# Optimization experiments

Measured on AMD Instinct MI355X. Metric: run time of the kernel, lower is better.

## Reference

```python
import jax, jax.numpy as jnp
import numpy as np

# TimeVaryingDelayLine forward (warmup=False path).
# The torch code builds an (N,C,T,max_delay+1) unfolded buffer and a triangular
# weight tensor relu(1 - |delay_axis - dt|). Since weights are a triangular hat of
# width 2, exactly two taps are nonzero: delay floor(dt) with weight (1-frac) and
# delay floor(dt)+1 with weight frac (frac = dt - floor(dt)). We compute the
# identical math with a direct fractional-index gather + lerp.

MAX_DELAY = 40000
CHANNELS = 2
BATCH = 8
T = 1_000_000

def setup_inputs() -> dict:
    key = jax.random.key(0)
    k1, k2 = jax.random.split(key)
    x = jax.random.normal(k1, (BATCH, CHANNELS, T), dtype=jnp.float32)
    # delays in samples, in [0, MAX_DELAY-1) so the +1 tap index stays in range
    dt = jax.random.uniform(k2, (BATCH, CHANNELS, T), dtype=jnp.float32) * (MAX_DELAY - 1)
    buffer = jnp.zeros((BATCH, CHANNELS, MAX_DELAY), dtype=jnp.float32)
    return {"x": x, "dt": dt, "buffer": buffer}

def reference(x, dt, buffer):
    max_delay = buffer.shape[2]
    n_samples = x.shape[2]
    # x_pad[..., max_delay + t] is the current sample t  -> shape (N, C, max_delay + T)
    x_pad = jnp.concatenate([buffer, x], axis=2)
    pos = max_delay + jnp.arange(n_samples, dtype=jnp.int32)  # (T,)
    i0 = jnp.floor(dt).astype(jnp.int32)          # integer part of delay
    frac = dt - i0.astype(dt.dtype)               # fractional part in [0,1)
    idx0 = pos[None, None, :] - i0                # tap at delay floor(dt)
    idx1 = jnp.maximum(idx0 - 1, 0)               # tap at delay floor(dt)+1 (clipped; weight 0 at edge)
    tap0 = jnp.take_along_axis(x_pad, idx0, axis=2)
    tap1 = jnp.take_along_axis(x_pad, idx1, axis=2)
    y = (1.0 - frac) * tap0 + frac * tap1
    return y
```

## Files before the change

kernel.cpp:

```cpp
#include <hip/hip_runtime.h>
#include <stdint.h>


#define MAX_DELAY 40000
#define T_LEN     1000000
#define XPAD      (MAX_DELAY + T_LEN)
#define CHUNK     8192
#define S_ELEMS   16384
#define S_BYTES   (S_ELEMS * 4)
#define NPASS     3
#define CPS       123
#define NXCD      8

typedef __attribute__((address_space(3))) uint32_t       lds_u32;
typedef const __attribute__((address_space(1))) uint32_t glb_u32;

__global__ __launch_bounds__(256, 2) void tvdl_kernel(
    const float* __restrict__ x,
    const float* __restrict__ dt,
    const float* __restrict__ buf,
    float* __restrict__ y,
    int chunk_per_xcd)
{
    __shared__ float lds[S_ELEMS];

    int bid = blockIdx.x;
    int lb  = (bid & (NXCD - 1)) * chunk_per_xcd + (bid >> 3);
    int nc  = lb / CPS;
    int c   = lb - nc * CPS;
    int t0  = c * CHUNK;
    int tid = threadIdx.x;

    const float* __restrict__ xs  = x   + (size_t)nc * T_LEN;
    const float* __restrict__ bs  = buf + (size_t)nc * MAX_DELAY;
    const float* __restrict__ dts = dt  + (size_t)nc * T_LEN;
    float*       __restrict__ ys  = y   + (size_t)nc * T_LEN;

    int   b1[8][4];
    float fr[8][4];
    float acc[8][4];

#pragma unroll
    for (int k = 0; k < 8; ++k) {
        int go   = (k * 256 + tid) * 4;
        int lidx = t0 + go;
        int lc   = lidx > T_LEN - 4 ? T_LEN - 4 : lidx;
        float4 d4 = *reinterpret_cast<const float4*>(dts + lc);
        float dv[4] = {d4.x, d4.y, d4.z, d4.w};
#pragma unroll
        for (int j = 0; j < 4; ++j) {
            float dvj = dv[j];
            int   i0  = (int)dvj;
            fr[k][j]  = dvj - (float)i0;
            b1[k][j]  = (MAX_DELAY - 1 + (go + j) - i0) * 4;
            acc[k][j] = 0.0f;
        }
    }

#pragma unroll
    for (int p = 0; p < NPASS; ++p) {
#pragma unroll
        for (int q = 0; q < 16; ++q) {
            int g = t0 + p * S_ELEMS + (q * 256 + tid) * 4;
            if (g > XPAD - 4) g = XPAD - 4;
            const float* src = (g >= MAX_DELAY) ? (xs + (g - MAX_DELAY))
                                                : (bs + g);
            float* dst = lds + (size_t)(q * 256 + (tid & 192)) * 4;
            __builtin_amdgcn_global_load_lds((glb_u32*)src, (lds_u32*)dst, 16, 0, 0);
        }
        __syncthreads();

#pragma unroll
        for (int k = 0; k < 8; ++k) {
#pragma unroll
            for (int j = 0; j < 4; ++j) {
                int      bb = b1[k][j] - p * S_BYTES;
                unsigned ub = (unsigned)bb;
                if (ub < (unsigned)(S_BYTES - 4)) {
                    const float* lp = (const float*)((const char*)lds + ub);
                    float t1v = lp[0];
                    float t0v = lp[1];
                    float f   = fr[k][j];
                    acc[k][j] = fmaf(1.0f - f, t0v, fmaf(f, t1v, acc[k][j]));
                } else if (ub == (unsigned)(S_BYTES - 4)) {
                    acc[k][j] = fmaf(fr[k][j], lds[S_ELEMS - 1], acc[k][j]);
                } else if (bb == -4) {
                    acc[k][j] = fmaf(1.0f - fr[k][j], lds[0], acc[k][j]);
                }
            }
        }

        if (p + 1 < NPASS) __syncthreads();
    }

#pragma unroll
    for (int k = 0; k < 8; ++k) {
        int go = (k * 256 + tid) * 4;
        if (t0 + go < T_LEN) {
            *reinterpret_cast<float4*>(ys + t0 + go) =
                make_float4(acc[k][0], acc[k][1], acc[k][2], acc[k][3]);
        }
    }
}

extern "C" void kernel_launch(void* const* d_in, const int* in_sizes, int n_in,
                              void* d_out, int out_size, void* d_ws, size_t ws_size,
                              hipStream_t stream) {
    const float* x   = (const float*)d_in[0];
    const float* dt  = (const float*)d_in[1];
    const float* buf = (const float*)d_in[2];
    float* y = (float*)d_out;

    int nseries = out_size / T_LEN;
    int blocks  = nseries * CPS;
    int chunk_per_xcd = blocks / NXCD;
    tvdl_kernel<<<blocks, 256, 0, stream>>>(x, dt, buf, y, chunk_per_xcd);
}
```

Before: 82.18 us.

## Double-buffer LDS staging to overlap next window load with tap gathering

Splits the 64KB LDS window into two 32KB buffers and doubles the number of passes to six. The next window is issued with async global-to-LDS loads while the current window is gathered and interpolated, so memory latency can hide behind LDS work. In exchange, each pass still checks all 32 taps per thread, so the per-pass bounds tests and branching double. There are also more barriers.

```diff
diff --git a/kernel.cpp b/kernel.cpp
--- a/kernel.cpp
+++ b/kernel.cpp
@@ -6,9 +6,9 @@
 #define T_LEN     1000000
 #define XPAD      (MAX_DELAY + T_LEN)
 #define CHUNK     8192
-#define S_ELEMS   16384
+#define S_ELEMS   8192
 #define S_BYTES   (S_ELEMS * 4)
-#define NPASS     3
+#define NPASS     6
 #define CPS       123
 #define NXCD      8
 
@@ -22,7 +22,7 @@
     float* __restrict__ y,
     int chunk_per_xcd)
 {
-    __shared__ float lds[S_ELEMS];
+    __shared__ float lds[2][S_ELEMS];
 
     int bid = blockIdx.x;
     int lb  = (bid & (NXCD - 1)) * chunk_per_xcd + (bid >> 3);
@@ -57,19 +57,29 @@
         }
     }
 
+#define STAGE(b, p)                                                          \
+    {                                                                        \
+        _Pragma("unroll")                                                    \
+        for (int q = 0; q < 8; ++q) {                                        \
+            int g = t0 + (p) * S_ELEMS + (q * 256 + tid) * 4;                \
+            if (g > XPAD - 4) g = XPAD - 4;                                  \
+            const float* src = (g >= MAX_DELAY) ? (xs + (g - MAX_DELAY))     \
+                                                : (bs + g);                  \
+            float* dst = lds[b] + (size_t)(q * 256 + (tid & 192)) * 4;       \
+            __builtin_amdgcn_global_load_lds((glb_u32*)src, (lds_u32*)dst,   \
+                                             16, 0, 0);                      \
+        }                                                                    \
+    }
+
+    STAGE(0, 0);
+    __syncthreads();
+
 #pragma unroll
     for (int p = 0; p < NPASS; ++p) {
-#pragma unroll
-        for (int q = 0; q < 16; ++q) {
-            int g = t0 + p * S_ELEMS + (q * 256 + tid) * 4;
-            if (g > XPAD - 4) g = XPAD - 4;
-            const float* src = (g >= MAX_DELAY) ? (xs + (g - MAX_DELAY))
-                                                : (bs + g);
-            float* dst = lds + (size_t)(q * 256 + (tid & 192)) * 4;
-            __builtin_amdgcn_global_load_lds((glb_u32*)src, (lds_u32*)dst, 16, 0, 0);
-        }
-        __syncthreads();
+        const int cur = p & 1;
+        if (p + 1 < NPASS) STAGE(cur ^ 1, p + 1);
 
+        const float* lb0 = lds[cur];
 #pragma unroll
         for (int k = 0; k < 8; ++k) {
 #pragma unroll
@@ -77,21 +87,22 @@
                 int      bb = b1[k][j] - p * S_BYTES;
                 unsigned ub = (unsigned)bb;
                 if (ub < (unsigned)(S_BYTES - 4)) {
-                    const float* lp = (const float*)((const char*)lds + ub);
+                    const float* lp = (const float*)((const char*)lb0 + ub);
                     float t1v = lp[0];
                     float t0v = lp[1];
                     float f   = fr[k][j];
                     acc[k][j] = fmaf(1.0f - f, t0v, fmaf(f, t1v, acc[k][j]));
                 } else if (ub == (unsigned)(S_BYTES - 4)) {
-                    acc[k][j] = fmaf(fr[k][j], lds[S_ELEMS - 1], acc[k][j]);
+                    acc[k][j] = fmaf(fr[k][j], lb0[S_ELEMS - 1], acc[k][j]);
                 } else if (bb == -4) {
-                    acc[k][j] = fmaf(1.0f - fr[k][j], lds[0], acc[k][j]);
+                    acc[k][j] = fmaf(1.0f - fr[k][j], lb0[0], acc[k][j]);
                 }
             }
         }
 
         if (p + 1 < NPASS) __syncthreads();
     }
+#undef STAGE
 
 #pragma unroll
     for (int k = 0; k < 8; ++k) {
```

Result: slower. 131.9 us (+60.5%).
